# Optimization experiments

Hardware: AMD Instinct MI355X
Metric: run time of the kernel (lower is better)

The kernel has to match this reference:

```python
import jax, jax.numpy as jnp
import numpy as np

B, S, D_IN, D_Q, D_V, H = 2, 2048, 1024, 1024, 1024, 16
HD_Q, HD_V = D_Q // H, D_V // H
SCALE = float(D_Q) ** 0.5  # source scales by sqrt(d_q), NOT sqrt(head_dim)


def setup_inputs() -> dict:
    key = jax.random.key(0)
    k1, k2, k3, k4, k5 = jax.random.split(key, 5)
    return {
        "x": jax.random.normal(k1, (B, S, D_IN), dtype=jnp.float32),
        "w_q": jax.random.normal(k2, (D_IN, D_Q), dtype=jnp.float32),
        "w_k": jax.random.normal(k3, (D_IN, D_Q), dtype=jnp.float32),
        "w_v": jax.random.normal(k4, (D_IN, D_V), dtype=jnp.float32),
        "W_o": jax.random.normal(k5, (D_IN, D_V), dtype=jnp.float32),
    }


def reference(x, w_q, w_k, w_v, W_o):
    b, s, _ = x.shape
    # projections: [b, s, d]
    q = x @ w_q
    k = x @ w_k
    v = x @ w_v
    # split heads -> [b, h, s, hd]
    Q = q.reshape(b, s, H, HD_Q).transpose(0, 2, 1, 3)
    K = k.reshape(b, s, H, HD_Q).transpose(0, 2, 1, 3)
    V = v.reshape(b, s, H, HD_V).transpose(0, 2, 1, 3)
    # full [b, h, s, s] score matrix (naive attention, as in source)
    scores = jnp.einsum("bhqd,bhkd->bhqk", Q, K)
    # FAITHFUL QUIRK: source applies softmax over dim=0 (batch axis)
    attn = jax.nn.softmax(scores / SCALE, axis=0)
    vals = jnp.einsum("bhqk,bhkd->bhqd", attn, V)
    vals = vals.transpose(0, 2, 1, 3).reshape(b, s, D_V)
    return vals @ W_o
```

## Files before the change

### kernel.cpp

```cpp
#include <hip/hip_runtime.h>


typedef _Float16 f16;
typedef __attribute__((ext_vector_type(8))) _Float16 f16x8;
typedef __attribute__((ext_vector_type(4))) _Float16 f16x4;
typedef __attribute__((ext_vector_type(4))) float f32x4;

#define MFMA16(a,b,c)  __builtin_amdgcn_mfma_f32_16x16x32_f16(a,b,c,0,0,0)
#define MFMA16K(a,b,c) __builtin_amdgcn_mfma_f32_16x16x16f16(a,b,c,0,0,0)
#define GLD16(gp, lp) __builtin_amdgcn_global_load_lds(                         \
    (const __attribute__((address_space(1))) void*)(gp),                        \
    (__attribute__((address_space(3))) void*)(lp), 16, 0, 0)

__global__ __launch_bounds__(256) void prep(const float* __restrict__ x,
                                            const float* __restrict__ w0, const float* __restrict__ w1,
                                            const float* __restrict__ w2, const float* __restrict__ w3,
                                            f16* __restrict__ xh,
                                            f16* __restrict__ o0, f16* __restrict__ o1,
                                            f16* __restrict__ o2, f16* __restrict__ o3) {
    const int bb = blockIdx.x;
    const int tid = threadIdx.x;
    if (bb >= 1024) {
        int i = (bb - 1024) * 256 + tid;
        float4 v = ((const float4*)x)[i];
        f16x4 h;
        h[0] = (f16)v.x; h[1] = (f16)v.y; h[2] = (f16)v.z; h[3] = (f16)v.w;
        *(f16x4*)(xh + (long)i * 4) = h;
        return;
    }
    const float* w; f16* o;
    switch (bb & 3) {
        case 0: w = w0; o = o0; break;
        case 1: w = w1; o = o1; break;
        case 2: w = w2; o = o2; break;
        default: w = w3; o = o3; break;
    }
    __shared__ alignas(16) f16 t[64][72];
    const int d0 = ((bb >> 2) & 15) * 64, j0 = (bb >> 6) * 64;
    #pragma unroll
    for (int it = 0; it < 4; ++it) {
        int idx = it * 256 + tid;
        int row = idx >> 4, c4 = idx & 15;
        float4 v = *(const float4*)(w + (long)(d0 + row) * 1024 + j0 + c4 * 4);
        f16x4 h;
        h[0] = (f16)v.x; h[1] = (f16)v.y; h[2] = (f16)v.z; h[3] = (f16)v.w;
        *(f16x4*)&t[row][c4 * 4] = h;
    }
    __syncthreads();
    #pragma unroll
    for (int it = 0; it < 4; ++it) {
        int idx = it * 256 + tid;
        int jr = idx >> 4, d4 = idx & 15;
        f16x4 h;
        #pragma unroll
        for (int m = 0; m < 4; ++m) h[m] = t[d4 * 4 + m][jr];
        *(f16x4*)(o + (long)(j0 + jr) * 1024 + d0 + d4 * 4) = h;
    }
}

__global__ __launch_bounds__(256, 1) void gemm_qkv(const f16* __restrict__ A,
                                                   const f16* __restrict__ Wt,
                                                   f16* __restrict__ Qg,
                                                   f16* __restrict__ Kg,
                                                   f16* __restrict__ Vtg) {
    __shared__ alignas(16) f16 smem[16384];
    f16* As = smem;
    f16* Bs = smem + 8192;
    const int tid = threadIdx.x;
    const int wave = tid >> 6, lane = tid & 63;
    const int l15 = lane & 15, lq = lane >> 4;
    const int sw = l15 & 7;
    const int m0 = blockIdx.x * 128, n0 = blockIdx.y * 128;
    const int wr = (wave >> 1) * 64, wc = (wave & 1) * 64;
    const int r8 = lane >> 3;
    const int swc8 = ((lane & 7) ^ r8) * 8;

    f32x4 acc[4][4] = {};

    for (int kt = 0; kt < 16; ++kt) {
        __syncthreads();
        #pragma unroll
        for (int i = 0; i < 4; ++i) {
            GLD16(A  + (long)(m0 + wave * 32 + i * 8 + r8) * 1024 + kt * 64 + swc8, As + (wave * 32 + i * 8) * 64);
            GLD16(Wt + (long)(n0 + wave * 32 + i * 8 + r8) * 1024 + kt * 64 + swc8, Bs + (wave * 32 + i * 8) * 64);
        }
        __syncthreads();
        #pragma unroll
        for (int s2 = 0; s2 < 2; ++s2) {
            const int rc = ((s2 * 4 + lq) ^ sw) << 3;
            f16x8 af[4], bf[4];
            #pragma unroll
            for (int i = 0; i < 4; ++i) af[i] = *(const f16x8*)&As[(wr + i * 16 + l15) * 64 + rc];
            #pragma unroll
            for (int j = 0; j < 4; ++j) bf[j] = *(const f16x8*)&Bs[(wc + j * 16 + l15) * 64 + rc];
            #pragma unroll
            for (int i = 0; i < 4; ++i)
                #pragma unroll
                for (int j = 0; j < 4; ++j)
                    acc[i][j] = MFMA16(af[i], bf[j], acc[i][j]);
        }
    }

    const int sel = n0 >> 10;
    const int nb = n0 - (sel << 10);

    if (sel < 2) {
        f16* dst = sel == 0 ? Qg : Kg;
        const float qs = sel == 0 ? 0.045084219f : 1.0f;
        __syncthreads();
        #pragma unroll
        for (int i = 0; i < 4; ++i)
            #pragma unroll
            for (int j = 0; j < 4; ++j) {
                int row0 = wr + i * 16 + lq * 4;
                int colb = wc + j * 16 + l15;
                int chunk = colb >> 3, sub = colb & 7;
                #pragma unroll
                for (int r = 0; r < 4; ++r) {
                    int row = row0 + r;
                    smem[row * 128 + ((chunk ^ (row & 7)) << 3) + sub] = (f16)(acc[i][j][r] * qs);
                }
            }
        __syncthreads();
        #pragma unroll
        for (int e = 0; e < 8; ++e) {
            int id = e * 256 + tid;
            int row = id >> 4, c = id & 15;
            f16x8 v = *(const f16x8*)&smem[row * 128 + ((c ^ (row & 7)) << 3)];
            int gr = m0 + row, b = gr >> 11, s = gr & 2047;
            int gc = nb + c * 8, hh = gc >> 6, hd = gc & 63;
            *(f16x8*)(dst + (long)((b * 16 + hh) * 2048 + s) * 64 + hd) = v;
        }
    } else {
        #pragma unroll
        for (int i = 0; i < 4; ++i)
            #pragma unroll
            for (int j = 0; j < 4; ++j) {
                int gr0 = m0 + wr + i * 16 + lq * 4;
                int gc  = nb + wc + j * 16 + l15;
                int b = gr0 >> 11, s = gr0 & 2047;
                int hh = gc >> 6, hd = gc & 63;
                f16x4 v;
                #pragma unroll
                for (int r = 0; r < 4; ++r) v[r] = (f16)acc[i][j][r];
                *(f16x4*)(Vtg + (long)((b * 16 + hh) * 64 + hd) * 2048 + s) = v;
            }
    }
}

template<int NSUM>
__global__ __launch_bounds__(256, 1) void gemm_out(const f16* __restrict__ A0,
                                                   const f16* __restrict__ A1,
                                                   const f16* __restrict__ A2,
                                                   const f16* __restrict__ A3,
                                                   const f16* __restrict__ Bt,
                                                   float* __restrict__ outp) {
    __shared__ alignas(16) f16 As[64][72];
    __shared__ alignas(16) f16 Bs[128][64];
    const int tid = threadIdx.x;
    const int wave = tid >> 6, lane = tid & 63;
    const int l15 = lane & 15, lq = lane >> 4;
    const int sw = l15 & 7;
    const int m0 = blockIdx.x * 64, n0 = blockIdx.y * 128;
    const int wr = (wave >> 1) * 32, wc = (wave & 1) * 64;
    const int r8 = lane >> 3;
    const int swc8 = ((lane & 7) ^ r8) * 8;

    f32x4 acc[2][4] = {};

    for (int kt = 0; kt < 16; ++kt) {
        __syncthreads();
        #pragma unroll
        for (int it = 0; it < 2; ++it) {
            int idx = it * 256 + tid;
            int row = idx >> 3, c = idx & 7;
            long off = (long)(m0 + row) * 1024 + kt * 64 + c * 8;
            f16x8 a = *(const f16x8*)(A0 + off) + *(const f16x8*)(A1 + off);
            if constexpr (NSUM == 4)
                a = a + *(const f16x8*)(A2 + off) + *(const f16x8*)(A3 + off);
            *(f16x8*)&As[row][c * 8] = a;
        }
        #pragma unroll
        for (int i = 0; i < 4; ++i)
            GLD16(Bt + (long)(n0 + wave * 32 + i * 8 + r8) * 1024 + kt * 64 + swc8, &Bs[wave * 32 + i * 8][0]);
        __syncthreads();
        #pragma unroll
        for (int s2 = 0; s2 < 2; ++s2) {
            const int rc = ((s2 * 4 + lq) ^ sw) << 3;
            f16x8 af[2], bf[4];
            #pragma unroll
            for (int i = 0; i < 2; ++i) af[i] = *(const f16x8*)&As[wr + i * 16 + l15][s2 * 32 + lq * 8];
            #pragma unroll
            for (int j = 0; j < 4; ++j) bf[j] = *(const f16x8*)&Bs[wc + j * 16 + l15][rc];
            #pragma unroll
            for (int i = 0; i < 2; ++i)
                #pragma unroll
                for (int j = 0; j < 4; ++j)
                    acc[i][j] = MFMA16(af[i], bf[j], acc[i][j]);
        }
    }

    #pragma unroll
    for (int i = 0; i < 2; ++i)
        #pragma unroll
        for (int j = 0; j < 4; ++j) {
            int gr0 = m0 + wr + i * 16 + lq * 4;
            int gc  = n0 + wc + j * 16 + l15;
            #pragma unroll
            for (int r = 0; r < 4; ++r)
                outp[(long)(gr0 + r) * 1024 + gc] = acc[i][j][r];
        }
}

__global__ __launch_bounds__(256, 3) void attention_kernel(const f16* __restrict__ Qg,
                                                           const f16* __restrict__ Kg,
                                                           const f16* __restrict__ Vtg,
                                                           f16* __restrict__ v0,
                                                           f16* __restrict__ v1,
                                                           f16* __restrict__ v2,
                                                           f16* __restrict__ v3) {
    __shared__ alignas(16) f16 Ks [2][2][32][64];
    __shared__ alignas(16) f16 Vts[2][2][64][32];
    const int tid = threadIdx.x;
    const int wave = tid >> 6, lane = tid & 63;
    const int l15 = lane & 15, lq = lane >> 4;
    const int sw  = l15 & 7;

    const int NS = gridDim.x >> 8;
    const int nt = 64 / NS;
    const int bid = blockIdx.x;
    const int xcd = bid & 7, sl = bid >> 3;
    const int h  = xcd * 2 + (sl & 1);
    const int qt = (sl >> 1) & 15, ks = sl >> 5;
    const int q0 = qt * 128;
    const int key0 = ks * (nt << 5);
    f16* vals = ks == 0 ? v0 : ks == 1 ? v1 : ks == 2 ? v2 : v3;
    const int qr = q0 + wave * 32;

    f16x8 qfr[2][2][2];
    #pragma unroll
    for (int b2 = 0; b2 < 2; ++b2)
        #pragma unroll
        for (int qq = 0; qq < 2; ++qq)
            #pragma unroll
            for (int s2 = 0; s2 < 2; ++s2)
                qfr[b2][qq][s2] = *(const f16x8*)(Qg + (long)((b2 * 16 + h) * 2048 + qr + qq * 16 + l15) * 64
                                                  + s2 * 32 + lq * 8);

    f32x4 acc[2][2][4] = {};

    const int tb = wave & 1;
    const int r8 = lane >> 3;
    const int swc8 = ((lane & 7) ^ r8) * 8;
    const f16* kbase = Kg  + (long)((tb * 16 + h) * 2048 + key0) * 64 + r8 * 64 + swc8;
    const f16* vbase = Vtg + (long)((tb * 16 + h) * 64 + (lane >> 2)) * 2048 + key0
                       + ((lane & 3) ^ ((lane >> 2) & 3)) * 8;

    auto stage = [&](int kt, int buf) {
        if (wave < 2) {
            const f16* g = kbase + kt * 2048;
            f16* l = &Ks[buf][tb][0][0];
            #pragma unroll
            for (int i = 0; i < 4; ++i) GLD16(g + i * 512, l + i * 512);
        } else {
            const f16* g = vbase + kt * 32;
            f16* l = &Vts[buf][tb][0][0];
            #pragma unroll
            for (int i = 0; i < 4; ++i) GLD16(g + (long)i * 16 * 2048, l + i * 512);
        }
    };

    const int vro = l15 * 32 + (lq & 1) * 4 + ((((lq >> 1) ^ (l15 & 3))) << 3);
    const f16* VtsF = &Vts[0][0][0][0];

    stage(0, 0);
    for (int kt = 0; kt < nt; ++kt) {
        const int cur = kt & 1;
        __syncthreads();
        if (kt < nt - 1) stage(kt + 1, cur ^ 1);

        f16x4 pp0[2][2], pp1[2][2];
        #pragma unroll
        for (int kf = 0; kf < 2; ++kf) {
            f32x4 S0[2] = {}, S1[2] = {};
            __builtin_amdgcn_s_setprio(1);
            #pragma unroll
            for (int s2 = 0; s2 < 2; ++s2) {
                const int rc = ((s2 * 4 + lq) ^ sw) << 3;
                f16x8 a0 = *(const f16x8*)&Ks[cur][0][kf * 16 + l15][rc];
                f16x8 a1 = *(const f16x8*)&Ks[cur][1][kf * 16 + l15][rc];
                #pragma unroll
                for (int qq = 0; qq < 2; ++qq) {
                    S0[qq] = MFMA16(a0, qfr[0][qq][s2], S0[qq]);
                    S1[qq] = MFMA16(a1, qfr[1][qq][s2], S1[qq]);
                }
            }
            __builtin_amdgcn_s_setprio(0);
            #pragma unroll
            for (int qq = 0; qq < 2; ++qq) {
                f16x4 p0v;
                #pragma unroll
                for (int r = 0; r < 4; ++r) {
                    float e = __builtin_amdgcn_exp2f(S1[qq][r] - S0[qq][r]);
                    float p = __builtin_amdgcn_rcpf(1.0f + e);
                    p0v[r] = (f16)p;
                }
                f16x4 onev = {(f16)1.f, (f16)1.f, (f16)1.f, (f16)1.f};
                pp0[kf][qq] = p0v;
                pp1[kf][qq] = onev - p0v;
            }
        }

        #pragma unroll
        for (int pb = 0; pb < 2; ++pb) {
            #pragma unroll
            for (int kf = 0; kf < 2; ++kf) {
                f16x4 vfrag[4];
                #pragma unroll
                for (int hf = 0; hf < 4; ++hf)
                    vfrag[hf] = *(const f16x4*)&VtsF[cur * 4096 + pb * 2048 + hf * 512
                                                     + (vro ^ (kf << 4))];
                __builtin_amdgcn_s_setprio(1);
                #pragma unroll
                for (int qq = 0; qq < 2; ++qq)
                    #pragma unroll
                    for (int hf = 0; hf < 4; ++hf)
                        acc[pb][qq][hf] = MFMA16K(vfrag[hf],
                                                  pb ? pp1[kf][qq] : pp0[kf][qq],
                                                  acc[pb][qq][hf]);
                __builtin_amdgcn_s_setprio(0);
            }
        }
    }

    #pragma unroll
    for (int pb = 0; pb < 2; ++pb)
        #pragma unroll
        for (int qq = 0; qq < 2; ++qq)
            #pragma unroll
            for (int hf = 0; hf < 4; ++hf) {
                f16x4 ov;
                #pragma unroll
                for (int r = 0; r < 4; ++r) ov[r] = (f16)acc[pb][qq][hf][r];
                *(f16x4*)(vals + (long)(pb * 2048 + qr + qq * 16 + l15) * 1024
                          + h * 64 + hf * 16 + lq * 4) = ov;
            }
}

extern "C" void kernel_launch(void* const* d_in, const int* in_sizes, int n_in,
                              void* d_out, int out_size, void* d_ws, size_t ws_size,
                              hipStream_t stream) {
    const float* x  = (const float*)d_in[0];
    const float* wq = (const float*)d_in[1];
    const float* wk = (const float*)d_in[2];
    const float* wv = (const float*)d_in[3];
    const float* wo = (const float*)d_in[4];

    char* ws = (char*)d_ws;
    f16* xh    = (f16*)(ws);
    f16* wqT   = (f16*)(ws + 8388608);
    f16* wkT   = (f16*)(ws + 10485760);
    f16* wvT   = (f16*)(ws + 12582912);
    f16* woT   = (f16*)(ws + 14680064);
    f16* Qg    = (f16*)(ws + 16777216);
    f16* Kg    = (f16*)(ws + 25165824);
    f16* Vtg   = (f16*)(ws + 33554432);
    f16* vals1 = (f16*)(ws + 41943040);
    f16* vals2 = (f16*)(ws + 50331648);
    f16* vals3 = (f16*)(ws + 58720256);
    f16* vals0 = xh;
    (void)in_sizes; (void)n_in; (void)out_size;

    const int NS = (ws_size >= (size_t)67108864) ? 4 : 2;

    prep<<<5120, 256, 0, stream>>>(x, wq, wk, wv, wo, xh, wqT, wkT, wvT, woT);

    gemm_qkv<<<dim3(32, 24), 256, 0, stream>>>(xh, wqT, Qg, Kg, Vtg);

    attention_kernel<<<NS * 256, 256, 0, stream>>>(Qg, Kg, Vtg, vals0, vals1, vals2, vals3);

    if (NS == 4)
        gemm_out<4><<<dim3(64, 8), 256, 0, stream>>>(vals0, vals1, vals2, vals3, woT, (float*)d_out);
    else
        gemm_out<2><<<dim3(64, 8), 256, 0, stream>>>(vals0, vals1, vals0, vals0, woT, (float*)d_out);
}
```

Baseline: 201.1 us.

## Switch attention kernel to 32x32x16 MFMA with permlane-based P fragment repack

Rewrites the attention inner loop to use 32x32x16 f16 MFMA for both the QK^T scores and the P·V products, replacing the 16x16x32 and 16x16x16 tiles. The softmax probabilities are packed with cvt_pkrtz and rearranged across lane halves with v_permlane32_swap, so the score accumulator layout serves directly as the B operand of the PV MFMA. The V LDS swizzle and fragment addressing change to match. The aim is fewer MFMA issues and LDS reads per key tile, paid for with larger 16-float accumulators and more register pressure, which could hurt occupancy.

```diff
diff --git a/kernel.cpp b/kernel.cpp
--- a/kernel.cpp
+++ b/kernel.cpp
@@ -5,9 +5,10 @@
 typedef __attribute__((ext_vector_type(8))) _Float16 f16x8;
 typedef __attribute__((ext_vector_type(4))) _Float16 f16x4;
 typedef __attribute__((ext_vector_type(4))) float f32x4;
+typedef __attribute__((ext_vector_type(16))) float f32x16;
 
 #define MFMA16(a,b,c)  __builtin_amdgcn_mfma_f32_16x16x32_f16(a,b,c,0,0,0)
-#define MFMA16K(a,b,c) __builtin_amdgcn_mfma_f32_16x16x16f16(a,b,c,0,0,0)
+#define MFMA32(a,b,c)  __builtin_amdgcn_mfma_f32_32x32x16_f16(a,b,c,0,0,0)
 #define GLD16(gp, lp) __builtin_amdgcn_global_load_lds(                         \
     (const __attribute__((address_space(1))) void*)(gp),                        \
     (__attribute__((address_space(3))) void*)(lp), 16, 0, 0)
@@ -223,8 +224,9 @@
     __shared__ alignas(16) f16 Vts[2][2][64][32];
     const int tid = threadIdx.x;
     const int wave = tid >> 6, lane = tid & 63;
-    const int l15 = lane & 15, lq = lane >> 4;
-    const int sw  = l15 & 7;
+    const int l31 = lane & 31, hi = lane >> 5;
+    const int kchunk = l31 & 7;
+    const int vcb = (l31 >> 1) & 3;
 
     const int NS = gridDim.x >> 8;
     const int nt = 64 / NS;
@@ -237,24 +239,22 @@
     f16* vals = ks == 0 ? v0 : ks == 1 ? v1 : ks == 2 ? v2 : v3;
     const int qr = q0 + wave * 32;
 
-    f16x8 qfr[2][2][2];
+    f16x8 qfr[2][4];
     #pragma unroll
     for (int b2 = 0; b2 < 2; ++b2)
         #pragma unroll
-        for (int qq = 0; qq < 2; ++qq)
-            #pragma unroll
-            for (int s2 = 0; s2 < 2; ++s2)
-                qfr[b2][qq][s2] = *(const f16x8*)(Qg + (long)((b2 * 16 + h) * 2048 + qr + qq * 16 + l15) * 64
-                                                  + s2 * 32 + lq * 8);
-
-    f32x4 acc[2][2][4] = {};
+        for (int s2 = 0; s2 < 4; ++s2)
+            qfr[b2][s2] = *(const f16x8*)(Qg + (long)((b2 * 16 + h) * 2048 + qr + l31) * 64
+                                          + s2 * 16 + hi * 8);
+
+    f32x16 acc[2][2] = {};
 
     const int tb = wave & 1;
     const int r8 = lane >> 3;
     const int swc8 = ((lane & 7) ^ r8) * 8;
     const f16* kbase = Kg  + (long)((tb * 16 + h) * 2048 + key0) * 64 + r8 * 64 + swc8;
     const f16* vbase = Vtg + (long)((tb * 16 + h) * 64 + (lane >> 2)) * 2048 + key0
-                       + ((lane & 3) ^ ((lane >> 2) & 3)) * 8;
+                       + ((lane & 3) ^ ((lane >> 3) & 3)) * 8;
 
     auto stage = [&](int kt, int buf) {
         if (wave < 2) {
@@ -270,8 +270,8 @@
         }
     };
 
-    const int vro = l15 * 32 + (lq & 1) * 4 + ((((lq >> 1) ^ (l15 & 3))) << 3);
     const f16* VtsF = &Vts[0][0][0][0];
+    const f16x8 ones8 = {(f16)1.f,(f16)1.f,(f16)1.f,(f16)1.f,(f16)1.f,(f16)1.f,(f16)1.f,(f16)1.f};
 
     stage(0, 0);
     for (int kt = 0; kt < nt; ++kt) {
@@ -279,71 +279,69 @@
         __syncthreads();
         if (kt < nt - 1) stage(kt + 1, cur ^ 1);
 
-        f16x4 pp0[2][2], pp1[2][2];
-        #pragma unroll
-        for (int kf = 0; kf < 2; ++kf) {
-            f32x4 S0[2] = {}, S1[2] = {};
-            __builtin_amdgcn_s_setprio(1);
-            #pragma unroll
-            for (int s2 = 0; s2 < 2; ++s2) {
-                const int rc = ((s2 * 4 + lq) ^ sw) << 3;
-                f16x8 a0 = *(const f16x8*)&Ks[cur][0][kf * 16 + l15][rc];
-                f16x8 a1 = *(const f16x8*)&Ks[cur][1][kf * 16 + l15][rc];
-                #pragma unroll
-                for (int qq = 0; qq < 2; ++qq) {
-                    S0[qq] = MFMA16(a0, qfr[0][qq][s2], S0[qq]);
-                    S1[qq] = MFMA16(a1, qfr[1][qq][s2], S1[qq]);
+        f32x16 S0 = {}, S1 = {};
+        __builtin_amdgcn_s_setprio(1);
+        #pragma unroll
+        for (int s2 = 0; s2 < 4; ++s2) {
+            const int rc = ((s2 * 2 + hi) ^ kchunk) << 3;
+            f16x8 a0 = *(const f16x8*)&Ks[cur][0][l31][rc];
+            f16x8 a1 = *(const f16x8*)&Ks[cur][1][l31][rc];
+            S0 = MFMA32(a0, qfr[0][s2], S0);
+            S1 = MFMA32(a1, qfr[1][s2], S1);
+        }
+        __builtin_amdgcn_s_setprio(0);
+
+        unsigned pk[8];
+        #pragma unroll
+        for (int p = 0; p < 8; ++p) {
+            float e0 = __builtin_amdgcn_exp2f(S1[2 * p]     - S0[2 * p]);
+            float e1 = __builtin_amdgcn_exp2f(S1[2 * p + 1] - S0[2 * p + 1]);
+            float pa = __builtin_amdgcn_rcpf(1.0f + e0);
+            float pb = __builtin_amdgcn_rcpf(1.0f + e1);
+            auto h2 = __builtin_amdgcn_cvt_pkrtz(pa, pb);
+            pk[p] = __builtin_bit_cast(unsigned, h2);
+        }
+
+        f16x8 pf0[2], pf1[2];
+        #pragma unroll
+        for (int keyh = 0; keyh < 2; ++keyh) {
+            unsigned a0 = pk[4 * keyh + 0], b0 = pk[4 * keyh + 2];
+            unsigned a1 = pk[4 * keyh + 1], b1 = pk[4 * keyh + 3];
+            asm("v_permlane32_swap_b32 %0, %1" : "+v"(a0), "+v"(b0));
+            asm("v_permlane32_swap_b32 %0, %1" : "+v"(a1), "+v"(b1));
+            union { unsigned u[4]; f16x8 v; } m;
+            m.u[0] = a0; m.u[1] = a1; m.u[2] = b0; m.u[3] = b1;
+            pf0[keyh] = m.v;
+            pf1[keyh] = ones8 - m.v;
+        }
+
+        __builtin_amdgcn_s_setprio(1);
+        #pragma unroll
+        for (int pb = 0; pb < 2; ++pb)
+            #pragma unroll
+            for (int keyh = 0; keyh < 2; ++keyh) {
+                const f16x8 pfr = pb ? pf1[keyh] : pf0[keyh];
+                #pragma unroll
+                for (int hdh = 0; hdh < 2; ++hdh) {
+                    f16x8 vf = *(const f16x8*)&VtsF[cur * 4096 + pb * 2048 + hdh * 1024
+                                                    + l31 * 32 + (((keyh * 2 + hi) ^ vcb) << 3)];
+                    acc[pb][hdh] = MFMA32(vf, pfr, acc[pb][hdh]);
                 }
             }
-            __builtin_amdgcn_s_setprio(0);
-            #pragma unroll
-            for (int qq = 0; qq < 2; ++qq) {
-                f16x4 p0v;
-                #pragma unroll
-                for (int r = 0; r < 4; ++r) {
-                    float e = __builtin_amdgcn_exp2f(S1[qq][r] - S0[qq][r]);
-                    float p = __builtin_amdgcn_rcpf(1.0f + e);
-                    p0v[r] = (f16)p;
-                }
-                f16x4 onev = {(f16)1.f, (f16)1.f, (f16)1.f, (f16)1.f};
-                pp0[kf][qq] = p0v;
-                pp1[kf][qq] = onev - p0v;
-            }
-        }
-
-        #pragma unroll
-        for (int pb = 0; pb < 2; ++pb) {
-            #pragma unroll
-            for (int kf = 0; kf < 2; ++kf) {
-                f16x4 vfrag[4];
-                #pragma unroll
-                for (int hf = 0; hf < 4; ++hf)
-                    vfrag[hf] = *(const f16x4*)&VtsF[cur * 4096 + pb * 2048 + hf * 512
-                                                     + (vro ^ (kf << 4))];
-                __builtin_amdgcn_s_setprio(1);
-                #pragma unroll
-                for (int qq = 0; qq < 2; ++qq)
-                    #pragma unroll
-                    for (int hf = 0; hf < 4; ++hf)
-                        acc[pb][qq][hf] = MFMA16K(vfrag[hf],
-                                                  pb ? pp1[kf][qq] : pp0[kf][qq],
-                                                  acc[pb][qq][hf]);
-                __builtin_amdgcn_s_setprio(0);
-            }
-        }
+        __builtin_amdgcn_s_setprio(0);
     }
 
     #pragma unroll
     for (int pb = 0; pb < 2; ++pb)
         #pragma unroll
-        for (int qq = 0; qq < 2; ++qq)
-            #pragma unroll
-            for (int hf = 0; hf < 4; ++hf) {
+        for (int hdh = 0; hdh < 2; ++hdh)
+            #pragma unroll
+            for (int g = 0; g < 4; ++g) {
                 f16x4 ov;
                 #pragma unroll
-                for (int r = 0; r < 4; ++r) ov[r] = (f16)acc[pb][qq][hf][r];
-                *(f16x4*)(vals + (long)(pb * 2048 + qr + qq * 16 + l15) * 1024
-                          + h * 64 + hf * 16 + lq * 4) = ov;
+                for (int r2 = 0; r2 < 4; ++r2) ov[r2] = (f16)acc[pb][hdh][g * 4 + r2];
+                *(f16x4*)(vals + (long)(pb * 2048 + qr + l31) * 1024
+                          + h * 64 + hdh * 32 + g * 8 + hi * 4) = ov;
             }
 }
 
```

New measurement: 194.0 us. 1.04x faster.
